# Performance work log

Hardware: AMD Instinct MI355X
Metric: run time of the kernel (lower is better)

The kernel has to match this reference:

```python
import jax, jax.numpy as jnp
import numpy as np

N = 100_000      # nodes
E = 3_200_000    # edges (avg degree 32)
G = 1_000        # graphs (100 nodes each)
F_IN, H1, H2 = 3, 64, 128
MD, NC = 32, 10


def setup_inputs() -> dict:
    key = jax.random.key(0)
    ks = jax.random.split(key, 10)
    x = jax.random.normal(ks[0], (N, F_IN), dtype=jnp.float32)
    edge_index = jax.random.randint(ks[1], (2, E), 0, N, dtype=jnp.int64)
    batch = (jnp.arange(N) // (N // G)).astype(jnp.int32)  # sorted segment ids, all graphs non-empty
    moment_vecs = jax.random.normal(ks[2], (G, MD), dtype=jnp.float32)
    W1 = jax.random.normal(ks[3], (F_IN, H1), dtype=jnp.float32) * (1.0 / np.sqrt(F_IN))
    b1 = jnp.zeros((H1,), dtype=jnp.float32)
    W2 = jax.random.normal(ks[4], (H1, H2), dtype=jnp.float32) * (1.0 / np.sqrt(H1))
    b2 = jnp.zeros((H2,), dtype=jnp.float32)
    Wc1 = jax.random.normal(ks[5], (H2 + MD, H1), dtype=jnp.float32) * (1.0 / np.sqrt(H2 + MD))
    bc1 = jnp.zeros((H1,), dtype=jnp.float32)
    Wc2 = jax.random.normal(ks[6], (H1, NC), dtype=jnp.float32) * (1.0 / np.sqrt(H1))
    bc2 = jnp.zeros((NC,), dtype=jnp.float32)
    return dict(x=x, edge_index=edge_index, batch=batch, moment_vecs=moment_vecs,
                W1=W1, b1=b1, W2=W2, b2=b2, Wc1=Wc1, bc1=bc1, Wc2=Wc2, bc2=bc2)


def gcn_conv(x, row, col, norm, W, b, num_nodes):
    # PyG GCNConv: h = x @ W; out[col] += norm * h[row]; out += b
    h = x @ W
    msg = h[row] * norm[:, None]                      # [E+N, out_dim] gather
    out = jax.ops.segment_sum(msg, col, num_segments=num_nodes)
    return out + b


def reference(x, edge_index, batch, moment_vecs, W1, b1, W2, b2, Wc1, bc1, Wc2, bc2):
    n = x.shape[0]
    loop = jnp.arange(n, dtype=edge_index.dtype)
    row = jnp.concatenate([edge_index[0], loop])      # self-loops appended
    col = jnp.concatenate([edge_index[1], loop])
    deg = jax.ops.segment_sum(jnp.ones_like(col, dtype=x.dtype), col, num_segments=n)
    dinv = jnp.where(deg > 0, jax.lax.rsqrt(deg), 0.0)
    norm = dinv[row] * dinv[col]                      # D^{-1/2} (A+I) D^{-1/2}

    h = jax.nn.relu(gcn_conv(x, row, col, norm, W1, b1, n))
    h = jax.nn.relu(gcn_conv(h, row, col, norm, W2, b2, n))

    # global_mean_pool over batch segments
    counts = jax.ops.segment_sum(jnp.ones((n,), dtype=h.dtype), batch, num_segments=G)
    pooled = jax.ops.segment_sum(h, batch, num_segments=G) / jnp.maximum(counts, 1.0)[:, None]

    # graph_ids == arange(G) -> identity gather of moment_vecs
    z = jnp.concatenate([pooled, moment_vecs], axis=1)
    z = jax.nn.relu(z @ Wc1 + bc1)
    return z @ Wc2 + bc2
```

## Files before the change

### kernel.cpp

```cpp
#include <hip/hip_runtime.h>
#include <hip/hip_fp16.h>

#define NNODES 100000
#define NEDGES 3200000
#define NGRAPH 1000
#define NPG    100
#define MDIM   32
#define NCDIM  10

#define CAP     48
#define OVF_CAP 4096

#define NPART   8
#define PSIZE   12500
#define FCHUNK  6250
#define FBLKS   (NEDGES / FCHUNK)

#define W_S2    0
#define W_CNT   4800064
#define W_DINV  4900064
#define W_XD4   5000064
#define W_A4    5400064
#define W_G1H   5800064
#define W_OVF   9000064
#define WS_FLOATS 9008257

__global__ __launch_bounds__(256) void k_fillbkt(const int* __restrict__ ei,
                                                 int* __restrict__ cnt,
                                                 int* __restrict__ slot2,
                                                 int* __restrict__ ovf) {
    int part  = blockIdx.x & (NPART - 1);
    int chunk = blockIdx.x >> 3;
    int base  = chunk * FCHUNK;
    int end   = base + FCHUNK;
    int clo   = part * PSIZE;
    int chi   = clo + PSIZE;
    for (int e = base + threadIdx.x; e < end; e += 256) {
        int c = ei[NEDGES + e];
        if (c >= clo && c < chi) {
            int r = ei[e];
            int idx = atomicAdd(&cnt[c], 1);
            if (idx < CAP) {
                slot2[c * CAP + idx] = r;
            } else {
                int o = atomicAdd(&ovf[0], 1);
                if (o < OVF_CAP) { ovf[1 + 2 * o] = r; ovf[2 + 2 * o] = c; }
            }
        }
    }
}

__global__ __launch_bounds__(256) void k_prep(const int* __restrict__ cnt,
                                              const float* __restrict__ x,
                                              float* __restrict__ dinv,
                                              float4* __restrict__ xd4) {
    int i = blockIdx.x * blockDim.x + threadIdx.x;
    if (i >= NNODES) return;
    float di = rsqrtf((float)cnt[i] + 1.0f);
    dinv[i] = di;
    xd4[i] = make_float4(x[3 * i], x[3 * i + 1], x[3 * i + 2], di);
}

__global__ void k_a(const int* __restrict__ cnt, const int* __restrict__ slot2,
                    const float4* __restrict__ xd4, float4* __restrict__ a4) {
    int i = blockIdx.x * blockDim.x + threadIdx.x;
    if (i >= NNODES) return;
    int d = min(cnt[i], CAP);
    int s = i * CAP;
    float ax = 0.f, ay = 0.f, az = 0.f;
    for (int k = 0; k < d; k += 8) {
        float4 xr[8];
        #pragma unroll
        for (int j = 0; j < 8; ++j) {
            int idx = slot2[s + k + j];
            xr[j] = xd4[(k + j < d) ? idx : 0];
        }
        #pragma unroll
        for (int j = 0; j < 8; ++j) {
            float u = (k + j < d) ? xr[j].w : 0.f;
            ax += u * xr[j].x; ay += u * xr[j].y; az += u * xr[j].z;
        }
    }
    float4 xi = xd4[i];
    float di = xi.w;
    a4[i] = make_float4(di * (ax + di * xi.x),
                        di * (ay + di * xi.y),
                        di * (az + di * xi.z), di);
}

__global__ void k_ovfA(const int* __restrict__ ovf, const float4* __restrict__ xd4,
                       const float* __restrict__ dinv, float* __restrict__ a4f) {
    int n = min(ovf[0], OVF_CAP);
    for (int k = threadIdx.x; k < n; k += 256) {
        int r = ovf[1 + 2 * k];
        int c = ovf[2 + 2 * k];
        float4 xr = xd4[r];
        float s = dinv[c] * xr.w;
        atomicAdd(&a4f[c * 4 + 0], s * xr.x);
        atomicAdd(&a4f[c * 4 + 1], s * xr.y);
        atomicAdd(&a4f[c * 4 + 2], s * xr.z);
    }
}

__global__ __launch_bounds__(256) void k_g1(const float4* __restrict__ a4,
                                            const float* __restrict__ W1,
                                            const float* __restrict__ b1,
                                            unsigned int* __restrict__ g1h) {
    int t = blockIdx.x * blockDim.x + threadIdx.x;
    int i = t >> 5, j = t & 31;
    if (i >= NNODES) return;
    float4 ai = a4[i];
    int f0 = 2 * j, f1 = f0 + 1;
    float h0 = fmaxf(ai.x * W1[f0] + ai.y * W1[64 + f0] + ai.z * W1[128 + f0] + b1[f0], 0.f);
    float h1 = fmaxf(ai.x * W1[f1] + ai.y * W1[64 + f1] + ai.z * W1[128 + f1] + b1[f1], 0.f);
    __half2 hv = __floats2half2_rn(ai.w * h0, ai.w * h1);
    g1h[t] = *(unsigned int*)&hv;
}

__global__ __launch_bounds__(256, 4) void k_fusedA(
    const int* __restrict__ cnt, const int* __restrict__ slot2,
    const int* __restrict__ ovf,
    const unsigned int* __restrict__ g1h, const float* __restrict__ dinv,
    const float* __restrict__ mv,
    const float* __restrict__ W2, const float* __restrict__ b2,
    const float* __restrict__ Wc1, const float* __restrict__ bc1,
    const float* __restrict__ Wc2, const float* __restrict__ bc2,
    float* __restrict__ out)
{
    __shared__ float aggh[NPG * 66];
    __shared__ float pools[4 * 128];
    __shared__ float zbuf[160];
    __shared__ float zz[64];

    int g = blockIdx.x;
    int t = threadIdx.x;
    int wb = t >> 6;
    int lane = t & 63;
    int h = lane >> 5;
    int j = lane & 31;

    for (int i = 0; i < 25; ++i) {
        int n = wb * 25 + i;
        int node = g * NPG + n;
        int s = node * CAP;
        int d = min(cnt[node], CAP);
        float acc0 = 0.f, acc1 = 0.f;
        for (int k0 = 0; k0 < d; k0 += 16) {
            int rr[8];
            #pragma unroll
            for (int jj = 0; jj < 8; ++jj) {
                int pos = k0 + 2 * jj + h;
                int v = slot2[s + pos];
                rr[jj] = (pos < d) ? v : 0;
            }
            #pragma unroll
            for (int jj = 0; jj < 8; ++jj) {
                unsigned int v = g1h[rr[jj] * 32 + j];
                float2 f = __half22float2(*(__half2*)&v);
                bool ok = (k0 + 2 * jj + h) < d;
                acc0 += ok ? f.x : 0.f;
                acc1 += ok ? f.y : 0.f;
            }
        }
        acc0 += __shfl_xor(acc0, 32);
        acc1 += __shfl_xor(acc1, 32);
        if (h == 0) {
            unsigned int sv = g1h[node * 32 + j];
            float2 sf = __half22float2(*(__half2*)&sv);
            float dc = dinv[node];
            *(float2*)&aggh[n * 66 + 2 * j] =
                make_float2(dc * (acc0 + sf.x), dc * (acc1 + sf.y));
        }
    }
    {
        int novf = min(ovf[0], OVF_CAP);
        int glo = g * NPG;
        for (int k = 0; k < novf; ++k) {
            int r = ovf[1 + 2 * k];
            int c = ovf[2 + 2 * k];
            int n = c - glo;
            if (n >= wb * 25 && n < wb * 25 + 25 && h == 0) {
                unsigned int v = g1h[r * 32 + j];
                float2 f = __half22float2(*(__half2*)&v);
                float dc = dinv[c];
                aggh[n * 66 + 2 * j]     += dc * f.x;
                aggh[n * 66 + 2 * j + 1] += dc * f.y;
            }
        }
    }

    float2 b2v = *(const float2*)&b2[2 * lane];
    float pool0 = 0.f, pool1 = 0.f;
    {
        float acc0[13], acc1[13];
        #pragma unroll
        for (int i = 0; i < 13; ++i) { acc0[i] = 0.f; acc1[i] = 0.f; }
        float2 wv0 = *(const float2*)&W2[2 * lane];
        float2 wv1 = *(const float2*)&W2[128 + 2 * lane];
        for (int f = 0; f < 64; ++f) {
            float2 wnx = (f + 2 < 64) ? *(const float2*)&W2[(f + 2) * 128 + 2 * lane] : wv0;
            #pragma unroll
            for (int i = 0; i < 13; ++i) {
                float rv = aggh[(wb * 25 + i) * 66 + f];
                acc0[i] += rv * wv0.x;
                acc1[i] += rv * wv0.y;
            }
            wv0 = wv1; wv1 = wnx;
        }
        #pragma unroll
        for (int i = 0; i < 13; ++i) {
            pool0 += fmaxf(acc0[i] + b2v.x, 0.f);
            pool1 += fmaxf(acc1[i] + b2v.y, 0.f);
        }
    }
    {
        float acc0[12], acc1[12];
        #pragma unroll
        for (int i = 0; i < 12; ++i) { acc0[i] = 0.f; acc1[i] = 0.f; }
        float2 wv0 = *(const float2*)&W2[2 * lane];
        float2 wv1 = *(const float2*)&W2[128 + 2 * lane];
        for (int f = 0; f < 64; ++f) {
            float2 wnx = (f + 2 < 64) ? *(const float2*)&W2[(f + 2) * 128 + 2 * lane] : wv0;
            #pragma unroll
            for (int i = 0; i < 12; ++i) {
                float rv = aggh[(wb * 25 + 13 + i) * 66 + f];
                acc0[i] += rv * wv0.x;
                acc1[i] += rv * wv0.y;
            }
            wv0 = wv1; wv1 = wnx;
        }
        #pragma unroll
        for (int i = 0; i < 12; ++i) {
            pool0 += fmaxf(acc0[i] + b2v.x, 0.f);
            pool1 += fmaxf(acc1[i] + b2v.y, 0.f);
        }
    }

    pools[wb * 128 + 2 * lane]     = pool0;
    pools[wb * 128 + 2 * lane + 1] = pool1;
    __syncthreads();
    if (t < 128)
        zbuf[t] = (pools[t] + pools[128 + t] + pools[256 + t] + pools[384 + t]) * (1.0f / NPG);
    if (t < MDIM) zbuf[128 + t] = mv[g * MDIM + t];
    __syncthreads();
    if (t < 64) {
        float v = bc1[t];
        for (int k = 0; k < 160; ++k) v += zbuf[k] * Wc1[k * 64 + t];
        zz[t] = fmaxf(v, 0.f);
    }
    __syncthreads();
    if (t < NCDIM) {
        float o = bc2[t];
        #pragma unroll
        for (int k = 0; k < 64; ++k) o += zz[k] * Wc2[k * NCDIM + t];
        out[g * NCDIM + t] = o;
    }
}

extern "C" void kernel_launch(void* const* d_in, const int* in_sizes, int n_in,
                              void* d_out, int out_size, void* d_ws, size_t ws_size,
                              hipStream_t stream) {
    const float* x   = (const float*)d_in[0];
    const int*   ei  = (const int*)d_in[1];
    const float* mv  = (const float*)d_in[3];
    const float* W1  = (const float*)d_in[4];
    const float* b1  = (const float*)d_in[5];
    const float* W2  = (const float*)d_in[6];
    const float* b2  = (const float*)d_in[7];
    const float* Wc1 = (const float*)d_in[8];
    const float* bc1 = (const float*)d_in[9];
    const float* Wc2 = (const float*)d_in[10];
    const float* bc2 = (const float*)d_in[11];
    float* out = (float*)d_out;
    float* ws  = (float*)d_ws;

    if (ws_size < (size_t)WS_FLOATS * sizeof(float)) return;

    int*          slot2  = (int*)(ws + W_S2);
    int*          cnt    = (int*)(ws + W_CNT);
    float*        dinv   = ws + W_DINV;
    float4*       xd4    = (float4*)(ws + W_XD4);
    float4*       a4     = (float4*)(ws + W_A4);
    unsigned int* g1h    = (unsigned int*)(ws + W_G1H);
    int*          ovf    = (int*)(ws + W_OVF);

    hipMemsetAsync(cnt, 0, (size_t)NNODES * sizeof(int), stream);
    hipMemsetAsync(ovf, 0, sizeof(int), stream);

    k_fillbkt<<<FBLKS * NPART, 256, 0, stream>>>(ei, cnt, slot2, ovf);
    k_prep   <<<(NNODES + 255) / 256, 256, 0, stream>>>(cnt, x, dinv, xd4);
    k_a      <<<(NNODES + 255) / 256, 256, 0, stream>>>(cnt, slot2, xd4, a4);
    k_ovfA   <<<1, 256, 0, stream>>>(ovf, xd4, dinv, (float*)a4);
    k_g1     <<<(NNODES * 32) / 256, 256, 0, stream>>>(a4, W1, b1, g1h);
    k_fusedA <<<NGRAPH, 256, 0, stream>>>(cnt, slot2, ovf, g1h, dinv, mv,
                                          W2, b2, Wc1, bc1, Wc2, bc2, out);
}
```

Measured before the change: 358.5 us.

## Split per-graph fused aggregation across two blocks and move MLP head to separate kernel

The fused layer-2 aggregation/pool kernel now launches two blocks per graph, each handling 50 nodes with an interleaved node-to-wave assignment, and writes partial pooled sums to workspace. A new small head kernel combines the two halves and runs the classifier MLP. The bucket-fill kernel also uses 4 column partitions instead of 8, halving the number of passes over the edge list at the cost of more atomic spread per block. The intent is better GPU occupancy with 2000 blocks and less redundant edge reading, in exchange for an extra launch and a global round-trip of pooled partials.

```diff
diff --git a/kernel.cpp b/kernel.cpp
--- a/kernel.cpp
+++ b/kernel.cpp
@@ -11,8 +11,8 @@
 #define CAP     48
 #define OVF_CAP 4096
 
-#define NPART   8
-#define PSIZE   12500
+#define NPART   4
+#define PSIZE   25000
 #define FCHUNK  6250
 #define FBLKS   (NEDGES / FCHUNK)
 
@@ -23,14 +23,15 @@
 #define W_A4    5400064
 #define W_G1H   5800064
 #define W_OVF   9000064
-#define WS_FLOATS 9008257
+#define W_PP    9008260
+#define WS_FLOATS 9264260
 
 __global__ __launch_bounds__(256) void k_fillbkt(const int* __restrict__ ei,
                                                  int* __restrict__ cnt,
                                                  int* __restrict__ slot2,
                                                  int* __restrict__ ovf) {
     int part  = blockIdx.x & (NPART - 1);
-    int chunk = blockIdx.x >> 3;
+    int chunk = blockIdx.x >> 2;
     int base  = chunk * FCHUNK;
     int end   = base + FCHUNK;
     int clo   = part * PSIZE;
@@ -121,27 +122,24 @@
     const int* __restrict__ cnt, const int* __restrict__ slot2,
     const int* __restrict__ ovf,
     const unsigned int* __restrict__ g1h, const float* __restrict__ dinv,
-    const float* __restrict__ mv,
     const float* __restrict__ W2, const float* __restrict__ b2,
-    const float* __restrict__ Wc1, const float* __restrict__ bc1,
-    const float* __restrict__ Wc2, const float* __restrict__ bc2,
-    float* __restrict__ out)
+    float* __restrict__ pp)
 {
-    __shared__ float aggh[NPG * 66];
+    __shared__ float aggh[50 * 66];
     __shared__ float pools[4 * 128];
-    __shared__ float zbuf[160];
-    __shared__ float zz[64];
-
-    int g = blockIdx.x;
+
+    int b = blockIdx.x;
+    int g = b >> 1, half = b & 1;
     int t = threadIdx.x;
     int wb = t >> 6;
     int lane = t & 63;
     int h = lane >> 5;
     int j = lane & 31;
-
-    for (int i = 0; i < 25; ++i) {
-        int n = wb * 25 + i;
-        int node = g * NPG + n;
+    int nn = (wb < 2) ? 13 : 12;
+
+    for (int i = 0; i < nn; ++i) {
+        int n = wb + 4 * i;
+        int node = g * NPG + half * 50 + n;
         int s = node * CAP;
         int d = min(cnt[node], CAP);
         float acc0 = 0.f, acc1 = 0.f;
@@ -174,12 +172,12 @@
     }
     {
         int novf = min(ovf[0], OVF_CAP);
-        int glo = g * NPG;
+        int glo = g * NPG + half * 50;
         for (int k = 0; k < novf; ++k) {
             int r = ovf[1 + 2 * k];
             int c = ovf[2 + 2 * k];
             int n = c - glo;
-            if (n >= wb * 25 && n < wb * 25 + 25 && h == 0) {
+            if (n >= 0 && n < 50 && (n & 3) == wb && h == 0) {
                 unsigned int v = g1h[r * 32 + j];
                 float2 f = __half22float2(*(__half2*)&v);
                 float dc = dinv[c];
@@ -190,57 +188,50 @@
     }
 
     float2 b2v = *(const float2*)&b2[2 * lane];
-    float pool0 = 0.f, pool1 = 0.f;
+    float acc0[13], acc1[13];
+    #pragma unroll
+    for (int i = 0; i < 13; ++i) { acc0[i] = 0.f; acc1[i] = 0.f; }
     {
-        float acc0[13], acc1[13];
-        #pragma unroll
-        for (int i = 0; i < 13; ++i) { acc0[i] = 0.f; acc1[i] = 0.f; }
         float2 wv0 = *(const float2*)&W2[2 * lane];
         float2 wv1 = *(const float2*)&W2[128 + 2 * lane];
         for (int f = 0; f < 64; ++f) {
             float2 wnx = (f + 2 < 64) ? *(const float2*)&W2[(f + 2) * 128 + 2 * lane] : wv0;
             #pragma unroll
             for (int i = 0; i < 13; ++i) {
-                float rv = aggh[(wb * 25 + i) * 66 + f];
+                float rv = (i < nn) ? aggh[(wb + 4 * i) * 66 + f] : 0.f;
                 acc0[i] += rv * wv0.x;
                 acc1[i] += rv * wv0.y;
             }
             wv0 = wv1; wv1 = wnx;
         }
-        #pragma unroll
-        for (int i = 0; i < 13; ++i) {
+    }
+    float pool0 = 0.f, pool1 = 0.f;
+    #pragma unroll
+    for (int i = 0; i < 13; ++i) {
+        if (i < nn) {
             pool0 += fmaxf(acc0[i] + b2v.x, 0.f);
             pool1 += fmaxf(acc1[i] + b2v.y, 0.f);
         }
     }
-    {
-        float acc0[12], acc1[12];
-        #pragma unroll
-        for (int i = 0; i < 12; ++i) { acc0[i] = 0.f; acc1[i] = 0.f; }
-        float2 wv0 = *(const float2*)&W2[2 * lane];
-        float2 wv1 = *(const float2*)&W2[128 + 2 * lane];
-        for (int f = 0; f < 64; ++f) {
-            float2 wnx = (f + 2 < 64) ? *(const float2*)&W2[(f + 2) * 128 + 2 * lane] : wv0;
-            #pragma unroll
-            for (int i = 0; i < 12; ++i) {
-                float rv = aggh[(wb * 25 + 13 + i) * 66 + f];
-                acc0[i] += rv * wv0.x;
-                acc1[i] += rv * wv0.y;
-            }
-            wv0 = wv1; wv1 = wnx;
-        }
-        #pragma unroll
-        for (int i = 0; i < 12; ++i) {
-            pool0 += fmaxf(acc0[i] + b2v.x, 0.f);
-            pool1 += fmaxf(acc1[i] + b2v.y, 0.f);
-        }
-    }
-
     pools[wb * 128 + 2 * lane]     = pool0;
     pools[wb * 128 + 2 * lane + 1] = pool1;
     __syncthreads();
     if (t < 128)
-        zbuf[t] = (pools[t] + pools[128 + t] + pools[256 + t] + pools[384 + t]) * (1.0f / NPG);
+        pp[b * 128 + t] = pools[t] + pools[128 + t] + pools[256 + t] + pools[384 + t];
+}
+
+__global__ __launch_bounds__(128) void k_head(
+    const float* __restrict__ pp, const float* __restrict__ mv,
+    const float* __restrict__ Wc1, const float* __restrict__ bc1,
+    const float* __restrict__ Wc2, const float* __restrict__ bc2,
+    float* __restrict__ out)
+{
+    __shared__ float zbuf[160];
+    __shared__ float zz[64];
+    int g = blockIdx.x;
+    int t = threadIdx.x;
+    if (t < 128)
+        zbuf[t] = (pp[(2 * g) * 128 + t] + pp[(2 * g + 1) * 128 + t]) * (1.0f / NPG);
     if (t < MDIM) zbuf[128 + t] = mv[g * MDIM + t];
     __syncthreads();
     if (t < 64) {
@@ -283,6 +274,7 @@
     float4*       a4     = (float4*)(ws + W_A4);
     unsigned int* g1h    = (unsigned int*)(ws + W_G1H);
     int*          ovf    = (int*)(ws + W_OVF);
+    float*        pp     = ws + W_PP;
 
     hipMemsetAsync(cnt, 0, (size_t)NNODES * sizeof(int), stream);
     hipMemsetAsync(ovf, 0, sizeof(int), stream);
@@ -292,6 +284,7 @@
     k_a      <<<(NNODES + 255) / 256, 256, 0, stream>>>(cnt, slot2, xd4, a4);
     k_ovfA   <<<1, 256, 0, stream>>>(ovf, xd4, dinv, (float*)a4);
     k_g1     <<<(NNODES * 32) / 256, 256, 0, stream>>>(a4, W1, b1, g1h);
-    k_fusedA <<<NGRAPH, 256, 0, stream>>>(cnt, slot2, ovf, g1h, dinv, mv,
-                                          W2, b2, Wc1, bc1, Wc2, bc2, out);
-}
+    k_fusedA <<<2 * NGRAPH, 256, 0, stream>>>(cnt, slot2, ovf, g1h, dinv,
+                                              W2, b2, pp);
+    k_head   <<<NGRAPH, 128, 0, stream>>>(pp, mv, Wc1, bc1, Wc2, bc2, out);
+}
```

New measurement: 454.4 us. +26.8%, slower.
